# Kernel tuning notes

Measured on AMD Instinct MI355X. Metric: run time of the kernel, lower is better.

## Reference

```python
import jax, jax.numpy as jnp
import numpy as np

NUM_HEAD = 16
D_Q = 512
D_KV = 512
ROPE_BASE = 10000.0


def _cos_sin(seq_len, dim):
    # Replicates calculate_cos_sin: theta = base**(-2*ids) / (dim//2)
    pos = jnp.arange(seq_len, dtype=jnp.float32)[:, None]          # (S,1)
    ids = jnp.arange(dim // 2, dtype=jnp.float32)                  # (D/2,)
    theta = (ROPE_BASE ** (-2.0 * ids)) / (dim // 2)
    r = pos * theta[None, :]                                       # (S, D/2)
    return jnp.cos(r), jnp.sin(r)


def _rope(x, cos, sin):
    b, s, d = x.shape
    xv = x.reshape(b, s, d // 2, 2)
    x0, x1 = xv[..., 0], xv[..., 1]
    out = jnp.stack([x0 * cos - x1 * sin, x1 * cos + x0 * sin], axis=-1)
    return out.reshape(b, s, d)


def setup_inputs() -> dict:
    key = jax.random.key(0)
    ks = jax.random.split(key, 10)
    d_model, d_q, d_kv = 1024, D_Q, D_KV
    b, s = 2, 2048
    w = lambda k, i, o: jax.random.normal(k, (i, o), dtype=jnp.float32) * 0.02
    return {
        "x": jax.random.normal(ks[0], (b, s, d_model), dtype=jnp.float32),
        "Wd_q_w": w(ks[1], d_model, d_q), "Wd_q_b": jnp.zeros((d_q,), jnp.float32),
        "Wu_q_w": w(ks[2], d_q, d_model), "Wu_q_b": jnp.zeros((d_model,), jnp.float32),
        "Wq_r_w": w(ks[3], d_q, d_model), "Wq_r_b": jnp.zeros((d_model,), jnp.float32),
        "Wk_r_w": w(ks[4], d_model, d_model), "Wk_r_b": jnp.zeros((d_model,), jnp.float32),
        "Wd_kv_w": w(ks[5], d_model, d_kv), "Wd_kv_b": jnp.zeros((d_kv,), jnp.float32),
        "Wu_k_w": w(ks[6], d_kv, d_model), "Wu_k_b": jnp.zeros((d_model,), jnp.float32),
        "Wu_v_w": w(ks[7], d_kv, d_model), "Wu_v_b": jnp.zeros((d_model,), jnp.float32),
        "Wo_w": w(ks[8], d_model, d_model), "Wo_b": jnp.zeros((d_model,), jnp.float32),
    }


def reference(x, Wd_q_w, Wd_q_b, Wu_q_w, Wu_q_b, Wq_r_w, Wq_r_b,
              Wk_r_w, Wk_r_b, Wd_kv_w, Wd_kv_b, Wu_k_w, Wu_k_b,
              Wu_v_w, Wu_v_b, Wo_w, Wo_b):
    b, s, d_model = x.shape
    h = NUM_HEAD
    hd = d_model // h
    scale = jnp.sqrt(jnp.float32(h + D_KV + D_Q))

    def heads(t):  # (b,s,d) -> (b,h,s,hd)
        return t.reshape(b, s, h, hd).transpose(0, 2, 1, 3)

    cos, sin = _cos_sin(s, d_model)

    ct_q = x @ Wd_q_w + Wd_q_b                                   # (b,s,d_q)
    qt_c = heads(ct_q @ Wu_q_w + Wu_q_b)
    qt_r = heads(_rope(ct_q @ Wq_r_w + Wq_r_b, cos, sin))
    query = qt_c + qt_r                                          # (b,h,s,hd)

    ct_kv = x @ Wd_kv_w + Wd_kv_b                                # (b,s,d_kv)
    kt_c = heads(ct_kv @ Wu_k_w + Wu_k_b)
    kt_r = heads(_rope(x @ Wk_r_w + Wk_r_b, cos, sin))
    key = kt_c + kt_r
    value = heads(ct_kv @ Wu_v_w + Wu_v_b)

    attn = jnp.einsum('bhqd,bhkd->bhqk', query, key) / scale
    attn = jax.nn.softmax(attn, axis=-1)
    out = jnp.einsum('bhqk,bhkd->bhqd', attn, value)
    out = out.transpose(0, 2, 1, 3).reshape(b, s, d_model)
    return out @ Wo_w + Wo_b
```

## Files before the change

### kernel.cpp

```cpp
#include <hip/hip_runtime.h>
#include <hip/hip_bf16.h>
#include <math.h>
#include <limits.h>

typedef __hip_bfloat16 bf16;
typedef __bf16 bf16x8 __attribute__((ext_vector_type(8)));
typedef float  f32x4  __attribute__((ext_vector_type(4)));

#define DEVI __device__ __forceinline__

static constexpr int Bb     = 2;
static constexpr int Ss     = 2048;
static constexpr int DMODEL = 1024;
static constexpr int NTOK   = Bb * Ss;

DEVI float bf2f(bf16 v) { return __bfloat162float(v); }
DEVI bf16  f2bf(float v) { return __float2bfloat16(v); }

DEVI unsigned int packbf(float lo, float hi) {
  union { bf16 b; unsigned short u; } a, c;
  a.b = f2bf(lo); c.b = f2bf(hi);
  return ((unsigned int)c.u << 16) | a.u;
}
DEVI float bfu2f(unsigned short u) {
  unsigned int x = (unsigned int)u << 16;
  float f; __builtin_memcpy(&f, &x, 4); return f;
}

DEVI void async_load16(const bf16* g, bf16* l) {
  __builtin_amdgcn_global_load_lds((const __attribute__((address_space(1))) void*)g,
                                   (__attribute__((address_space(3))) void*)l, 16, 0, 0);
}

struct TransDesc { const float* src; const float* src2; bf16* dst; int R; int C; int tstart; };
struct TransPack { TransDesc d[8]; };

__global__ __launch_bounds__(256) void trans_conv_kernel(
    TransPack p, const float* __restrict__ cx, bf16* __restrict__ cxo, int tstartConv,
    const float* __restrict__ ba1, const float* __restrict__ ba2,
    float* __restrict__ bsum, int tstartB) {
  __shared__ bf16 tl[64][65];
  const int t = blockIdx.x;
  if (t >= tstartB) {
    const int j = (t - tstartB) * 256 + threadIdx.x;
    bsum[j] = ba1[j] + ba2[j];
    return;
  }
  if (t >= tstartConv) {
    const int idx = (t - tstartConv) * 256 + threadIdx.x;
    const float4 v = ((const float4*)cx)[idx];
    uint2 o; o.x = packbf(v.x, v.y); o.y = packbf(v.z, v.w);
    *(uint2*)&cxo[(size_t)idx * 4] = o;
    return;
  }
  int i = 0;
#pragma unroll
  for (int j = 1; j < 8; ++j) if (t >= p.d[j].tstart) i = j;
  const float* __restrict__ in  = p.d[i].src;
  const float* __restrict__ in2 = p.d[i].src2;
  bf16* __restrict__ out = p.d[i].dst;
  const int R = p.d[i].R, C = p.d[i].C;
  const int rel = t - p.d[i].tstart;
  const int tilesC = C >> 6;
  const int r0 = (rel / tilesC) * 64, c0 = (rel % tilesC) * 64;
  const int tc = threadIdx.x & 63, tr = threadIdx.x >> 6;
#pragma unroll
  for (int q = 0; q < 16; ++q) {
    int r = tr + q * 4;
    float v = in[(size_t)(r0 + r) * C + c0 + tc];
    if (in2) v += in2[(size_t)(r0 + r) * C + c0 + tc];
    tl[r][tc] = f2bf(v);
  }
  __syncthreads();
#pragma unroll
  for (int q = 0; q < 16; ++q) {
    int r = tr + q * 4;
    out[(size_t)(c0 + r) * R + r0 + tc] = tl[tc][r];
  }
}

struct GemmDesc {
  const bf16* A; const bf16* WT; const float* b1; const float* b2; const bf16* addm; bf16* C;
  int lda, ldb, ldc, K, bsplit, nTX, blkStart, biasRow;
};
struct GemmBatch { GemmDesc d[4]; };

__global__ __launch_bounds__(256) void gemm_batch_kernel(GemmBatch gb) {
  const int t = blockIdx.x;
  int di = 0;
#pragma unroll
  for (int j = 1; j < 4; ++j) if (t >= gb.d[j].blkStart) di = j;
  const GemmDesc D = gb.d[di];
  const int rel = t - D.blkStart;
  const int tileN = (rel % D.nTX) * 128;
  const int tileM = (rel / D.nTX) * 128;

  __shared__ bf16 ldsA[128 * 32];
  __shared__ bf16 ldsB[128 * 32];
  const int tid = threadIdx.x;
  const int lane = tid & 63;
  const int w = tid >> 6;
  const int wr = w >> 1, wc = w & 1;
  const int l15 = lane & 15, lg = lane >> 4;
  const int lrow = lane >> 2;
  const int lcol = (lane & 3) * 8;

  f32x4 acc[4][4] = {};

  for (int k0 = 0; k0 < D.K; k0 += 32) {
    async_load16(D.A  + (size_t)(tileM + w * 32 +      lrow) * D.lda + k0 + lcol, &ldsA[(w * 32) * 32]);
    async_load16(D.A  + (size_t)(tileM + w * 32 + 16 + lrow) * D.lda + k0 + lcol, &ldsA[(w * 32 + 16) * 32]);
    async_load16(D.WT + (size_t)(tileN + w * 32 +      lrow) * D.ldb + k0 + lcol, &ldsB[(w * 32) * 32]);
    async_load16(D.WT + (size_t)(tileN + w * 32 + 16 + lrow) * D.ldb + k0 + lcol, &ldsB[(w * 32 + 16) * 32]);
    __syncthreads();

    bf16x8 af[4], bfr[4];
#pragma unroll
    for (int i = 0; i < 4; ++i) {
      af[i]  = *(const bf16x8*)&ldsA[(wr * 64 + i * 16 + l15) * 32 + lg * 8];
      bfr[i] = *(const bf16x8*)&ldsB[(wc * 64 + i * 16 + l15) * 32 + lg * 8];
    }
#pragma unroll
    for (int i = 0; i < 4; ++i)
#pragma unroll
      for (int j = 0; j < 4; ++j)
        acc[i][j] = __builtin_amdgcn_mfma_f32_16x16x32_bf16(af[i], bfr[j], acc[i][j], 0, 0, 0);
    __syncthreads();
  }

  const int mbase = tileM + wr * 64;
  const int nbase = tileN + wc * 64;
#pragma unroll
  for (int j = 0; j < 4; ++j) {
    int col = nbase + j * 16 + l15;
    float bvc = D.biasRow ? 0.0f : (col < D.bsplit ? D.b1[col] : D.b2[col - D.bsplit]);
    if (D.addm) {
      const int pcol = col >> 1;
      const bool odd = (col & 1) != 0;
#pragma unroll
      for (int i = 0; i < 4; ++i)
#pragma unroll
        for (int r = 0; r < 4; ++r) {
          int row = mbase + i * 16 + lg * 4 + r;
          unsigned int pr = *(const unsigned int*)((const char*)D.addm +
                              (size_t)row * D.ldc * 2 + (size_t)(col & ~1) * 2);
          float ke = bfu2f((unsigned short)(pr & 0xffff));
          float ko = bfu2f((unsigned short)(pr >> 16));
          float add;
          if (pcol == 0) {
            float rr = (float)(row & (Ss - 1)) * (1.0f / 512.0f);
            float c = cosf(rr), sn = sinf(rr);
            add = odd ? (ko * c + ke * sn) : (ke * c - ko * sn);
          } else {
            add = odd ? ko : ke;
          }
          D.C[(size_t)row * D.ldc + col] = f2bf(acc[i][j][r] + bvc + add);
        }
    } else {
#pragma unroll
      for (int i = 0; i < 4; ++i)
#pragma unroll
        for (int r = 0; r < 4; ++r) {
          int row = mbase + i * 16 + lg * 4 + r;
          float bv = D.biasRow ? D.b1[row] : bvc;
          D.C[(size_t)row * D.ldc + col] = f2bf(acc[i][j][r] + bv);
        }
    }
  }
}

__global__ __launch_bounds__(256) void gemm_kernel_f32(
    const bf16* __restrict__ A, int lda,
    const bf16* __restrict__ WT, int ldb,
    const float* __restrict__ b1,
    float* __restrict__ Cout, int ldc, int K) {
  __shared__ bf16 ldsA[128 * 32];
  __shared__ bf16 ldsB[64 * 32];
  const int tid = threadIdx.x;
  const int lane = tid & 63;
  const int w = tid >> 6;
  const int tileM = blockIdx.y * 128;
  const int tileN = blockIdx.x * 64;
  const int l15 = lane & 15, lg = lane >> 4;
  const int lrow = lane >> 2;
  const int lcol = (lane & 3) * 8;

  f32x4 acc[2][4] = {};

  for (int k0 = 0; k0 < K; k0 += 32) {
    async_load16(A  + (size_t)(tileM + w * 32 +      lrow) * lda + k0 + lcol, &ldsA[(w * 32) * 32]);
    async_load16(A  + (size_t)(tileM + w * 32 + 16 + lrow) * lda + k0 + lcol, &ldsA[(w * 32 + 16) * 32]);
    async_load16(WT + (size_t)(tileN + w * 16 + lrow) * ldb + k0 + lcol, &ldsB[(w * 16) * 32]);
    __syncthreads();

    bf16x8 af[2], bfr[4];
#pragma unroll
    for (int i = 0; i < 2; ++i)
      af[i]  = *(const bf16x8*)&ldsA[(w * 32 + i * 16 + l15) * 32 + lg * 8];
#pragma unroll
    for (int j = 0; j < 4; ++j)
      bfr[j] = *(const bf16x8*)&ldsB[(j * 16 + l15) * 32 + lg * 8];
#pragma unroll
    for (int i = 0; i < 2; ++i)
#pragma unroll
      for (int j = 0; j < 4; ++j)
        acc[i][j] = __builtin_amdgcn_mfma_f32_16x16x32_bf16(af[i], bfr[j], acc[i][j], 0, 0, 0);
    __syncthreads();
  }

#pragma unroll
  for (int j = 0; j < 4; ++j) {
    int col = tileN + j * 16 + l15;
    float bvc = b1[col];
#pragma unroll
    for (int i = 0; i < 2; ++i)
#pragma unroll
      for (int r = 0; r < 4; ++r) {
        int row = tileM + w * 32 + i * 16 + lg * 4 + r;
        Cout[(size_t)row * ldc + col] = acc[i][j][r] + bvc;
      }
  }
}

__global__ __launch_bounds__(256) void fixup_q_kernel(
    const bf16* __restrict__ ct, const float* __restrict__ Wqr,
    const float* __restrict__ Wqr_b, bf16* __restrict__ Q) {
  const int row = blockIdx.x * 4 + (threadIdx.x >> 6);
  const int lane = threadIdx.x & 63;
  const bf16* cr = ct + (size_t)row * 1024 + lane * 8;
  const float* wq = Wqr + (size_t)(lane * 8) * 1024;
  float q0 = 0.f, q1 = 0.f;
#pragma unroll
  for (int e = 0; e < 8; ++e) {
    float xv = bf2f(cr[e]);
    q0 = fmaf(xv, wq[e * 1024 + 0], q0);
    q1 = fmaf(xv, wq[e * 1024 + 1], q1);
  }
#pragma unroll
  for (int d = 32; d >= 1; d >>= 1) {
    q0 += __shfl_xor(q0, d, 64);
    q1 += __shfl_xor(q1, d, 64);
  }
  if (lane == 0) {
    const float Qr0 = q0 + Wqr_b[0], Qr1 = q1 + Wqr_b[1];
    const float rr = (float)(row & (Ss - 1)) * (1.0f / 512.0f);
    const float cm1 = cosf(rr) - 1.0f, sn = sinf(rr);
    const size_t base = (size_t)row * DMODEL;
    Q[base]     = f2bf(bf2f(Q[base])     + Qr0 * cm1 - Qr1 * sn);
    Q[base + 1] = f2bf(bf2f(Q[base + 1]) + Qr1 * cm1 + Qr0 * sn);
  }
}

__global__ __launch_bounds__(256) void attn_kernel(
    const bf16* __restrict__ Qm, const bf16* __restrict__ Kn,
    const bf16* __restrict__ VT, bf16* __restrict__ AO) {
  const int bh = blockIdx.x, qt = blockIdx.y;
  const int b = bh >> 4, h = bh & 15;
  const int tid = threadIdx.x, lane = tid & 63, w = tid >> 6;
  const int q0 = qt * 128 + w * 32;
  const int l15 = lane & 15, lg = lane >> 4;
  const float SC2 = 0.044736075f;
  const float THR = 11.5415603f;

  __shared__ bf16 ldsK[2][64 * 64];
  __shared__ bf16 ldsV[2][64 * 64];
  __shared__ bf16 ldsP[4][32 * 64];

  const bf16* Kg = Kn + (size_t)(b * Ss) * DMODEL + h * 64;
  const bf16* Vg = VT + (size_t)(h * 64) * NTOK + b * Ss;

  const int r0 = tid >> 3;
  const int srcb = ((tid & 7) * 16) ^ ((r0 & 7) << 4);
  const char* kS0 = (const char*)(Kg + (size_t)r0 * DMODEL) + srcb;
  const char* kS1 = (const char*)(Kg + (size_t)(32 + r0) * DMODEL) + srcb;
  const char* vS0 = (const char*)(Vg + (size_t)r0 * NTOK) + srcb;
  const char* vS1 = (const char*)(Vg + (size_t)(32 + r0) * NTOK) + srcb;
  const ptrdiff_t kAdv = (ptrdiff_t)64 * DMODEL * 2;
  const ptrdiff_t vAdv = 128;

  bf16* kd0_b0 = &ldsK[0][w * 512]; bf16* kd1_b0 = &ldsK[0][2048 + w * 512];
  bf16* kd0_b1 = &ldsK[1][w * 512]; bf16* kd1_b1 = &ldsK[1][2048 + w * 512];
  bf16* vd0_b0 = &ldsV[0][w * 512]; bf16* vd1_b0 = &ldsV[0][2048 + w * 512];
  bf16* vd0_b1 = &ldsV[1][w * 512]; bf16* vd1_b1 = &ldsV[1][2048 + w * 512];

  auto stageTo = [&](bf16* kd0, bf16* kd1, bf16* vd0, bf16* vd1) {
    async_load16((const bf16*)kS0, kd0);
    async_load16((const bf16*)kS1, kd1);
    async_load16((const bf16*)vS0, vd0);
    async_load16((const bf16*)vS1, vd1);
    kS0 += kAdv; kS1 += kAdv; vS0 += vAdv; vS1 += vAdv;
  };

  stageTo(kd0_b0, kd1_b0, vd0_b0, vd1_b0);

  const int kswz = (l15 & 7) << 4;
  const int xA = (lg * 16) ^ kswz;
  const int xB = (64 + lg * 16) ^ kswz;
  const char* krA0 = (const char*)&ldsK[0][0] + l15 * 128 + xA;
  const char* krB0 = (const char*)&ldsK[0][0] + l15 * 128 + xB;
  const char* krA1 = (const char*)&ldsK[1][0] + l15 * 128 + xA;
  const char* krB1 = (const char*)&ldsK[1][0] + l15 * 128 + xB;
  const char* vrA0 = (const char*)&ldsV[0][0] + l15 * 128 + xA;
  const char* vrB0 = (const char*)&ldsV[0][0] + l15 * 128 + xB;
  const char* vrA1 = (const char*)&ldsV[1][0] + l15 * 128 + xA;
  const char* vrB1 = (const char*)&ldsV[1][0] + l15 * 128 + xB;

  char* Pw = (char*)&ldsP[w][0];
  char* pwr[4];
#pragma unroll
  for (int j = 0; j < 4; ++j) {
    const int chunk = (j * 2 + (lg >> 1)) ^ (l15 & 7);
    pwr[j] = Pw + l15 * 128 + chunk * 16 + (lg & 1) * 8;
  }
  const char* paA = Pw + l15 * 128 + xA;
  const char* paB = Pw + l15 * 128 + xB;

  bf16x8 bq[2][2];
#pragma unroll
  for (int i = 0; i < 2; ++i) {
    const size_t rowoff = (size_t)(b * Ss + q0 + i * 16 + l15) * DMODEL + h * 64;
    bq[i][0] = *(const bf16x8*)&Qm[rowoff + lg * 8];
    bq[i][1] = *(const bf16x8*)&Qm[rowoff + 32 + lg * 8];
  }

  float m[2] = { 0.0f, 0.0f }, l[2] = { 0.0f, 0.0f };
  f32x4 accO[2][4] = {};

  auto body = [&](const char* krA, const char* krB, const char* vrA, const char* vrB) {
    f32x4 sa[4][2] = {};
    __builtin_amdgcn_s_setprio(1);
#pragma unroll
    for (int j = 0; j < 4; ++j) {
      bf16x8 ak0 = *(const bf16x8*)(krA + j * 2048);
      bf16x8 ak1 = *(const bf16x8*)(krB + j * 2048);
#pragma unroll
      for (int i = 0; i < 2; ++i) {
        sa[j][i] = __builtin_amdgcn_mfma_f32_16x16x32_bf16(ak0, bq[i][0], sa[j][i], 0, 0, 0);
        sa[j][i] = __builtin_amdgcn_mfma_f32_16x16x32_bf16(ak1, bq[i][1], sa[j][i], 0, 0, 0);
      }
    }
    __builtin_amdgcn_s_setprio(0);
#pragma unroll
    for (int i = 0; i < 2; ++i) {
      float pmaxr = -3.0e38f;
#pragma unroll
      for (int j = 0; j < 4; ++j)
#pragma unroll
        for (int r = 0; r < 4; ++r) pmaxr = fmaxf(pmaxr, sa[j][i][r]);
      if (__any(fmaf(pmaxr, SC2, -m[i]) > THR)) {
        float px = fmaxf(pmaxr, __shfl_xor(pmaxr, 16, 64));
        px = fmaxf(px, __shfl_xor(px, 32, 64));
        float mnew = fmaxf(m[i], px * SC2);
        float corr = __builtin_amdgcn_exp2f(m[i] - mnew);
        m[i] = mnew; l[i] *= corr;
        float cr[4];
#pragma unroll
        for (int r = 0; r < 4; ++r) cr[r] = __shfl(corr, lg * 4 + r, 64);
#pragma unroll
        for (int dj = 0; dj < 4; ++dj)
#pragma unroll
          for (int r = 0; r < 4; ++r) accO[i][dj][r] *= cr[r];
      }
      float p[4][4];
      float ts = 0.f;
#pragma unroll
      for (int j = 0; j < 4; ++j)
#pragma unroll
        for (int r = 0; r < 4; ++r) {
          p[j][r] = __builtin_amdgcn_exp2f(fmaf(sa[j][i][r], SC2, -m[i]));
          ts += p[j][r];
        }
      l[i] += ts;
#pragma unroll
      for (int j = 0; j < 4; ++j) {
        uint2 pw;
        pw.x = packbf(p[j][0], p[j][1]);
        pw.y = packbf(p[j][2], p[j][3]);
        *(uint2*)(pwr[j] + i * 2048) = pw;
      }
    }
    bf16x8 pa[2][2];
#pragma unroll
    for (int i = 0; i < 2; ++i) {
      pa[i][0] = *(const bf16x8*)(paA + i * 2048);
      pa[i][1] = *(const bf16x8*)(paB + i * 2048);
    }
    __builtin_amdgcn_s_setprio(1);
#pragma unroll
    for (int dj = 0; dj < 4; ++dj) {
      bf16x8 bv0 = *(const bf16x8*)(vrA + dj * 2048);
      bf16x8 bv1 = *(const bf16x8*)(vrB + dj * 2048);
#pragma unroll
      for (int i = 0; i < 2; ++i) {
        accO[i][dj] = __builtin_amdgcn_mfma_f32_16x16x32_bf16(pa[i][0], bv0, accO[i][dj], 0, 0, 0);
        accO[i][dj] = __builtin_amdgcn_mfma_f32_16x16x32_bf16(pa[i][1], bv1, accO[i][dj], 0, 0, 0);
      }
    }
    __builtin_amdgcn_s_setprio(0);
  };

  for (int tt = 0; tt < 16; ++tt) {
    __syncthreads();
    stageTo(kd0_b1, kd1_b1, vd0_b1, vd1_b1);
    body(krA0, krB0, vrA0, vrB0);
    __syncthreads();
    if (tt < 15) stageTo(kd0_b0, kd1_b0, vd0_b0, vd1_b0);
    body(krA1, krB1, vrA1, vrB1);
  }

#pragma unroll
  for (int i = 0; i < 2; ++i) {
    float lt = l[i];
    lt += __shfl_xor(lt, 16, 64);
    lt += __shfl_xor(lt, 32, 64);
    float linv[4];
#pragma unroll
    for (int r = 0; r < 4; ++r) linv[r] = 1.0f / __shfl(lt, lg * 4 + r, 64);
#pragma unroll
    for (int dj = 0; dj < 4; ++dj)
#pragma unroll
      for (int r = 0; r < 4; ++r)
        AO[(size_t)(b * Ss + q0 + i * 16 + lg * 4 + r) * DMODEL + h * 64 + dj * 16 + l15] =
            f2bf(accO[i][dj][r] * linv[r]);
  }
}

extern "C" void kernel_launch(void* const* d_in, const int* in_sizes, int n_in,
                              void* d_out, int out_size, void* d_ws, size_t ws_size,
                              hipStream_t stream) {
  const float* x      = (const float*)d_in[0];
  const float* Wdq    = (const float*)d_in[1];  const float* Wdq_b  = (const float*)d_in[2];
  const float* Wuq    = (const float*)d_in[3];  const float* Wuq_b  = (const float*)d_in[4];
  const float* Wqr    = (const float*)d_in[5];  const float* Wqr_b  = (const float*)d_in[6];
  const float* Wkr    = (const float*)d_in[7];  const float* Wkr_b  = (const float*)d_in[8];
  const float* Wdkv   = (const float*)d_in[9];  const float* Wdkv_b = (const float*)d_in[10];
  const float* Wuk    = (const float*)d_in[11]; const float* Wuk_b  = (const float*)d_in[12];
  const float* Wuv    = (const float*)d_in[13]; const float* Wuv_b  = (const float*)d_in[14];
  const float* Wo     = (const float*)d_in[15]; const float* Wo_b   = (const float*)d_in[16];

  char* ws = (char*)d_ws;
  size_t off = 0;
  bf16* WdqT   = (bf16*)(ws + off); off += (size_t)512  * 1024 * 2;
  bf16* WdkvT  = (bf16*)(ws + off); off += (size_t)512  * 1024 * 2;
  bf16* WuqqrT = (bf16*)(ws + off); off += (size_t)1024 * 512  * 2;
  bf16* WukT   = (bf16*)(ws + off); off += (size_t)1024 * 512  * 2;
  bf16* WuvT   = (bf16*)(ws + off); off += (size_t)1024 * 512  * 2;
  bf16* WkrT   = (bf16*)(ws + off); off += (size_t)1024 * 1024 * 2;
  bf16* WoT    = (bf16*)(ws + off); off += (size_t)1024 * 1024 * 2;
  bf16* x_bf   = (bf16*)(ws + off); off += (size_t)NTOK * 1024 * 2;
  bf16* ct     = (bf16*)(ws + off); off += (size_t)NTOK * 1024 * 2;
  bf16* Ga     = (bf16*)(ws + off); off += (size_t)NTOK * 1024 * 2;
  bf16* VTr    = (bf16*)(ws + off); off += (size_t)NTOK * 1024 * 2;
  float* qsum_b= (float*)(ws + off); off += 1024 * 4;
  bf16* Kn     = (bf16*)d_out + (size_t)NTOK * DMODEL;
  bf16* AO     = Ga;
  (void)ws_size; (void)in_sizes; (void)n_in; (void)out_size;

  TransPack tp = {{
    { Wdq,  0,   WdqT,   1024, 512,  0    },
    { Wdkv, 0,   WdkvT,  1024, 512,  128  },
    { Wuq,  Wqr, WuqqrT, 512,  1024, 256  },
    { Wuk,  0,   WukT,   512,  1024, 384  },
    { Wuv,  0,   WuvT,   512,  1024, 512  },
    { Wkr,  0,   WkrT,   1024, 1024, 640  },
    { Wo,   0,   WoT,    1024, 1024, 896  },
    { 0, 0, 0, 0, 0, 1 << 30 },
  }};
  trans_conv_kernel<<<1152 + 4096 + 4, 256, 0, stream>>>(
      tp, x, x_bf, 1152, Wuq_b, Wqr_b, qsum_b, 1152 + 4096);

  GemmBatch ba = {{
    { x_bf, WdqT, Wdq_b, Wdkv_b, 0, ct, 1024, 1024, 1024, 1024, 512,     8, 0,       0 },
    { x_bf, WkrT, Wkr_b, Wkr_b,  0, Kn, 1024, 1024, 1024, 1024, INT_MAX, 8, 256,     0 },
    { 0, 0, 0, 0, 0, 0, 0, 0, 0, 0, 0, 1, INT_MAX, 0 },
    { 0, 0, 0, 0, 0, 0, 0, 0, 0, 0, 0, 1, INT_MAX, 0 },
  }};
  gemm_batch_kernel<<<512, 256, 0, stream>>>(ba);

  GemmBatch bb = {{
    { ct,       WuqqrT,   qsum_b, qsum_b, 0,  Ga,  1024, 512,  1024, 512, INT_MAX, 8,  0,   0 },
    { ct + 512, WukT,     Wuk_b,  Wuk_b,  Kn, Kn,  1024, 512,  1024, 512, INT_MAX, 8,  256, 0 },
    { WuvT,     ct + 512, Wuv_b,  Wuv_b,  0,  VTr, 512,  1024, NTOK, 512, INT_MAX, 32, 512, 1 },
    { 0, 0, 0, 0, 0, 0, 0, 0, 0, 0, 0, 1, 1 << 30, 0 },
  }};
  gemm_batch_kernel<<<768, 256, 0, stream>>>(bb);

  fixup_q_kernel<<<NTOK / 4, 256, 0, stream>>>(ct, Wqr, Wqr_b, Ga);

  attn_kernel<<<dim3(32, 16), 256, 0, stream>>>(Ga, Kn, VTr, AO);

  gemm_kernel_f32<<<dim3(16, 32), 256, 0, stream>>>(
      AO, 1024, WoT, 1024, Wo_b, (float*)d_out, 1024, 1024);
}
```

Baseline: 168.0 us.

## Split attention KV range in two and merge partials with a combine kernel

Each attention block now handles half of the key/value sequence, which doubles the grid from 512 to 1024 blocks so more of the GPU's CUs are busy. Every half writes its unnormalized output in bf16 along with its per-row max and sum. A new combine kernel rescales and merges the two halves. This adds a kernel launch, extra global memory traffic for the partial outputs, and some bf16 rounding on the unnormalized partials.

```diff
diff --git a/kernel.cpp b/kernel.cpp
--- a/kernel.cpp
+++ b/kernel.cpp
@@ -253,8 +253,10 @@
 
 __global__ __launch_bounds__(256) void attn_kernel(
     const bf16* __restrict__ Qm, const bf16* __restrict__ Kn,
-    const bf16* __restrict__ VT, bf16* __restrict__ AO) {
-  const int bh = blockIdx.x, qt = blockIdx.y;
+    const bf16* __restrict__ VT, bf16* __restrict__ Op0, bf16* __restrict__ Op1,
+    float2* __restrict__ mlbuf) {
+  const int bh = blockIdx.x;
+  const int qt = blockIdx.y >> 1, sk = blockIdx.y & 1;
   const int b = bh >> 4, h = bh & 15;
   const int tid = threadIdx.x, lane = tid & 63, w = tid >> 6;
   const int q0 = qt * 128 + w * 32;
@@ -266,15 +268,17 @@
   __shared__ bf16 ldsV[2][64 * 64];
   __shared__ bf16 ldsP[4][32 * 64];
 
+  bf16* __restrict__ Opart = sk ? Op1 : Op0;
   const bf16* Kg = Kn + (size_t)(b * Ss) * DMODEL + h * 64;
   const bf16* Vg = VT + (size_t)(h * 64) * NTOK + b * Ss;
 
   const int r0 = tid >> 3;
   const int srcb = ((tid & 7) * 16) ^ ((r0 & 7) << 4);
-  const char* kS0 = (const char*)(Kg + (size_t)r0 * DMODEL) + srcb;
-  const char* kS1 = (const char*)(Kg + (size_t)(32 + r0) * DMODEL) + srcb;
-  const char* vS0 = (const char*)(Vg + (size_t)r0 * NTOK) + srcb;
-  const char* vS1 = (const char*)(Vg + (size_t)(32 + r0) * NTOK) + srcb;
+  const int kvbase = sk * 1024;
+  const char* kS0 = (const char*)(Kg + (size_t)(kvbase + r0) * DMODEL) + srcb;
+  const char* kS1 = (const char*)(Kg + (size_t)(kvbase + 32 + r0) * DMODEL) + srcb;
+  const char* vS0 = (const char*)(Vg + (size_t)r0 * NTOK + kvbase) + srcb;
+  const char* vS1 = (const char*)(Vg + (size_t)(32 + r0) * NTOK + kvbase) + srcb;
   const ptrdiff_t kAdv = (ptrdiff_t)64 * DMODEL * 2;
   const ptrdiff_t vAdv = 128;
 
@@ -399,12 +403,12 @@
     __builtin_amdgcn_s_setprio(0);
   };
 
-  for (int tt = 0; tt < 16; ++tt) {
+  for (int tt = 0; tt < 8; ++tt) {
     __syncthreads();
     stageTo(kd0_b1, kd1_b1, vd0_b1, vd1_b1);
     body(krA0, krB0, vrA0, vrB0);
     __syncthreads();
-    if (tt < 15) stageTo(kd0_b0, kd1_b0, vd0_b0, vd1_b0);
+    if (tt < 7) stageTo(kd0_b0, kd1_b0, vd0_b0, vd1_b0);
     body(krA1, krB1, vrA1, vrB1);
   }
 
@@ -413,16 +417,44 @@
     float lt = l[i];
     lt += __shfl_xor(lt, 16, 64);
     lt += __shfl_xor(lt, 32, 64);
-    float linv[4];
-#pragma unroll
-    for (int r = 0; r < 4; ++r) linv[r] = 1.0f / __shfl(lt, lg * 4 + r, 64);
+    if (lg == 0)
+      mlbuf[((size_t)sk * 32 + bh) * Ss + q0 + i * 16 + l15] = make_float2(m[i], lt);
 #pragma unroll
     for (int dj = 0; dj < 4; ++dj)
 #pragma unroll
       for (int r = 0; r < 4; ++r)
-        AO[(size_t)(b * Ss + q0 + i * 16 + lg * 4 + r) * DMODEL + h * 64 + dj * 16 + l15] =
-            f2bf(accO[i][dj][r] * linv[r]);
-  }
+        Opart[(size_t)(b * Ss + q0 + i * 16 + lg * 4 + r) * DMODEL + h * 64 + dj * 16 + l15] =
+            f2bf(accO[i][dj][r]);
+  }
+}
+
+__global__ __launch_bounds__(256) void combine_kernel(
+    const bf16* __restrict__ Op0, const bf16* __restrict__ Op1,
+    const float2* __restrict__ mlbuf, bf16* __restrict__ AO) {
+  const int t = blockIdx.x * blockDim.x + threadIdx.x;
+  const int row = t >> 7;
+  const int cg = t & 127;
+  const int h = cg >> 3;
+  const int b = row >> 11, q = row & (Ss - 1);
+  const size_t mlidx = ((size_t)(b * 16 + h)) * Ss + q;
+  const float2 ml0 = mlbuf[mlidx];
+  const float2 ml1 = mlbuf[(size_t)32 * Ss + mlidx];
+  const float M = fmaxf(ml0.x, ml1.x);
+  const float c0 = exp2f(ml0.x - M), c1 = exp2f(ml1.x - M);
+  const float linv = 1.0f / (ml0.y * c0 + ml1.y * c1);
+  const size_t off = (size_t)row * DMODEL + cg * 8;
+  union { bf16x8 v; unsigned short u[8]; } o0, o1;
+  o0.v = *(const bf16x8*)&Op0[off];
+  o1.v = *(const bf16x8*)&Op1[off];
+  uint4 o;
+  unsigned int* op = &o.x;
+#pragma unroll
+  for (int j = 0; j < 4; ++j) {
+    float a0 = (bfu2f(o0.u[2 * j])     * c0 + bfu2f(o1.u[2 * j])     * c1) * linv;
+    float a1 = (bfu2f(o0.u[2 * j + 1]) * c0 + bfu2f(o1.u[2 * j + 1]) * c1) * linv;
+    op[j] = packbf(a0, a1);
+  }
+  *(uint4*)&AO[off] = o;
 }
 
 extern "C" void kernel_launch(void* const* d_in, const int* in_sizes, int n_in,
@@ -452,7 +484,10 @@
   bf16* Ga     = (bf16*)(ws + off); off += (size_t)NTOK * 1024 * 2;
   bf16* VTr    = (bf16*)(ws + off); off += (size_t)NTOK * 1024 * 2;
   float* qsum_b= (float*)(ws + off); off += 1024 * 4;
+  float2* mlb  = (float2*)(ws + off); off += (size_t)2 * 32 * Ss * 8;
   bf16* Kn     = (bf16*)d_out + (size_t)NTOK * DMODEL;
+  bf16* Opart0 = x_bf;
+  bf16* Opart1 = ct;
   bf16* AO     = Ga;
   (void)ws_size; (void)in_sizes; (void)n_in; (void)out_size;
 
@@ -487,7 +522,9 @@
 
   fixup_q_kernel<<<NTOK / 4, 256, 0, stream>>>(ct, Wqr, Wqr_b, Ga);
 
-  attn_kernel<<<dim3(32, 16), 256, 0, stream>>>(Ga, Kn, VTr, AO);
+  attn_kernel<<<dim3(32, 32), 256, 0, stream>>>(Ga, Kn, VTr, Opart0, Opart1, mlb);
+
+  combine_kernel<<<NTOK * 128 / 256, 256, 0, stream>>>(Opart0, Opart1, mlb, AO);
 
   gemm_kernel_f32<<<dim3(16, 32), 256, 0, stream>>>(
       AO, 1024, WoT, 1024, Wo_b, (float*)d_out, 1024, 1024);
```

Measured after the change: 176.4 us. +5.0%, slower.
